# Kernel optimization log

Measured on AMD Instinct MI355X. Metric: run time of the kernel, lower is better.

## Reference

```python
import jax, jax.numpy as jnp
import numpy as np

MB, NK, DM, DT = 4096, 8, 1024, 128
EPS = 1e-3  # LayerNormalization eps, added to sigma OUTSIDE sqrt


def setup_inputs() -> dict:
    key = jax.random.key(0)
    ks = jax.random.split(key, 7)
    xav = lambda fan_in, fan_out: (2.0 / (fan_in + fan_out)) ** 0.5
    return {
        "q": jax.random.normal(ks[0], (MB, NK, DM), jnp.float32),
        "k": jax.random.normal(ks[1], (MB, NK, DM), jnp.float32),
        "v": jax.random.normal(ks[2], (MB, NK, DM), jnp.float32),
        "w_qs": jax.random.normal(ks[3], (NK, DM, DT), jnp.float32) * xav(DM, DT),
        "w_ks": jax.random.normal(ks[4], (NK, DM, DT), jnp.float32) * xav(DM, DT),
        "w_vs": jax.random.normal(ks[5], (NK, DM, DT), jnp.float32) * xav(DM, DT),
        # torch Linear: weight [out, in] = [NK*DM, NK*DT]
        "proj_w": jax.random.normal(ks[6], (NK * DM, NK * DT), jnp.float32) * xav(NK * DT, NK * DM),
        "proj_b": jnp.zeros((NK * DM,), jnp.float32),
        "gamma": jnp.ones((DM,), jnp.float32),
        "beta": jnp.zeros((DM,), jnp.float32),
    }


def reference(q, k, v, w_qs, w_ks, w_vs, proj_w, proj_b, gamma, beta):
    mb, nk, dm = q.shape
    dt = w_qs.shape[-1]
    residual = v

    # torch: q.view(n_kernel, mb, d_model) on contiguous [mb, nk, dm] == raw reshape
    q_s = jnp.einsum('nbd,ndt->nbt', q.reshape(nk, mb, dm), w_qs)  # [nk, mb, dt]
    k_s = jnp.einsum('nbd,ndt->nbt', k.reshape(nk, mb, dm), w_ks)
    v_s = jnp.einsum('nbd,ndt->nbt', v.reshape(nk, mb, dm), w_vs)

    # ScaledDotProductAttention on [nk*mb, 1, dt] -> scores [.,1,1]; softmax over
    # a singleton dim is identically 1, so output == v_s (faithful to source).
    temper = np.float32(np.sqrt(dm))
    scores = jnp.sum(q_s * k_s, axis=-1) / temper            # [nk, mb]
    attn = jax.nn.softmax(scores[:, :, None, None], axis=-1)  # [nk, mb, 1, 1] == 1.0
    out = attn[..., 0] * v_s                                  # [nk, mb, dt]
    attns = attn.reshape(nk * mb, 1, 1)

    # torch .view(mb, nk*dt) on the [nk, mb, dt]-contiguous buffer (raw reshape)
    outputs = out.reshape(mb, nk * dt)
    outputs = outputs @ proj_w.T + proj_b                     # [mb, nk*dm]
    z = outputs.reshape(mb, nk, dm) + residual

    # custom LayerNormalization: unbiased std, eps outside sqrt
    mu = jnp.mean(z, axis=-1, keepdims=True)
    sigma = jnp.std(z, axis=-1, keepdims=True, ddof=1)
    output = (z - mu) / (sigma + EPS) * gamma + beta
    return (output, attns)
```

## Files before the change

kernel.cpp:

```cpp
#include <hip/hip_runtime.h>
#include <cstdint>
#include <cstddef>

#define MB_   4096
#define NK_   8
#define DM_   1024
#define DT_   128

typedef __bf16 bf16;
typedef __bf16 bf16x8 __attribute__((ext_vector_type(8)));
typedef __bf16 bf16x4 __attribute__((ext_vector_type(4)));
typedef float  f32x4  __attribute__((ext_vector_type(4)));

__device__ __forceinline__ void gload_lds16(const void* g, void* l) {
  __builtin_amdgcn_global_load_lds(
      (__attribute__((address_space(1))) void*)g,
      (__attribute__((address_space(3))) void*)l,
      16, 0, 0);
}

__device__ __forceinline__ int hsw(int r) { return (r ^ (r >> 2)) & 3; }

__global__ void prep_pw_kernel(const float* __restrict__ pw, bf16* __restrict__ pwb) {
  size_t i = ((size_t)blockIdx.x * 256 + threadIdx.x) * 4;
  float4 f = *(const float4*)&pw[i];
  bf16x4 o = { (bf16)f.x, (bf16)f.y, (bf16)f.z, (bf16)f.w };
  *(bf16x4*)&pwb[i] = o;
}

__global__ void prep_wvt_kernel(const float* __restrict__ wvs, bf16* __restrict__ wvt) {
  int o = blockIdx.x * 256 + threadIdx.x;
  int d = o & 1023;
  int t = (o >> 10) & 127;
  int n = o >> 17;
  wvt[o] = (bf16)wvs[(size_t)n * 131072 + (size_t)d * 128 + t];
}

__global__ void fill_attns_kernel(float* __restrict__ out) {
  out[(size_t)33554432 + blockIdx.x * 256 + threadIdx.x] = 1.0f;
}

__global__ __launch_bounds__(256, 2) void gemm1_kernel(
    const float* __restrict__ vflat, const bf16* __restrict__ WvT,
    bf16* __restrict__ A2)
{
  __shared__ __align__(16) bf16 As[64 * 32];
  __shared__ __align__(16) bf16 Bs[128 * 32];
  const int tid  = threadIdx.x;
  const int wave = tid >> 6, lane = tid & 63;
  const int wm = wave >> 1, wn = wave & 1;
  const int n  = blockIdx.y;
  const int b0 = blockIdx.x * 64;

  const int r  = tid >> 2;
  const int hr = hsw(r);
  const int cs = (tid & 3) ^ hr;

  const float* ag = vflat + ((size_t)(n * MB_ + b0 + r)) * 1024 + (tid & 3) * 8;
  bf16* awr = As + r * 32 + cs * 8;
  const bf16* bg = WvT + (size_t)n * 131072 + (size_t)r * 1024 + cs * 8;
  char* bsb = (char*)Bs + wave * 1024;

  f32x4 acc[2][4] = {};
  const int krow = lane & 15;
  const int cch  = lane >> 4;
  const int swoff = ((cch ^ hsw(krow)) << 4);

  for (int kt = 0; kt < 32; ++kt) {
    const bf16* bptr = bg + kt * 32;
    gload_lds16(bptr,             bsb);
    gload_lds16(bptr + 64 * 1024, bsb + 4096);
    const float* aptr = ag + kt * 32;
    float4 f0 = *(const float4*)(aptr + 0);
    float4 f1 = *(const float4*)(aptr + 4);
    bf16x8 h0 = { (bf16)f0.x, (bf16)f0.y, (bf16)f0.z, (bf16)f0.w,
                  (bf16)f1.x, (bf16)f1.y, (bf16)f1.z, (bf16)f1.w };
    *(bf16x8*)awr = h0;
    __syncthreads();

    bf16x8 af[2], bfr[4];
    #pragma unroll
    for (int i = 0; i < 2; ++i)
      af[i] = *(const bf16x8*)((const char*)As + (wm * 32 + i * 16 + krow) * 64 + swoff);
    #pragma unroll
    for (int j = 0; j < 4; ++j)
      bfr[j] = *(const bf16x8*)((const char*)Bs + (wn * 64 + j * 16 + krow) * 64 + swoff);
    #pragma unroll
    for (int i = 0; i < 2; ++i)
      #pragma unroll
      for (int j = 0; j < 4; ++j)
        acc[i][j] = __builtin_amdgcn_mfma_f32_16x16x32_bf16(af[i], bfr[j], acc[i][j], 0, 0, 0);
    __syncthreads();
  }

  #pragma unroll
  for (int i = 0; i < 2; ++i) {
    #pragma unroll
    for (int j = 0; j < 4; ++j) {
      int t = wn * 64 + j * 16 + (lane & 15);
      #pragma unroll
      for (int rr = 0; rr < 4; ++rr) {
        int b = b0 + wm * 32 + i * 16 + (lane >> 4) * 4 + rr;
        size_t off = ((size_t)(n * 512 + (b >> 3))) * 1024 + (size_t)(b & 7) * 128 + t;
        A2[off] = (bf16)acc[i][j][rr];
      }
    }
  }
}

template<bool ZB>
__global__ __launch_bounds__(512, 2) void gemm2p_kernel(
    const bf16* __restrict__ A2, const bf16* __restrict__ PW,
    const float* __restrict__ pb, void* __restrict__ zoutp)
{
  __shared__ __align__(16) bf16 As[4][8192];
  __shared__ __align__(16) bf16 Bs[4][8192];

  const int tid  = threadIdx.x;
  const int w    = tid >> 6;
  const int lane = tid & 63;
  const int wm   = w >> 2;
  const int wn   = w & 3;

  const int bid   = blockIdx.x;
  const int x     = bid & 7;
  const int local = bid >> 3;
  const int mt    = local & 15;
  const int nt    = x * 4 + (local >> 4);
  const int m0    = mt * 256;
  const int n0    = nt * 256;

  const char* aG0 = (const char*)A2 + (size_t)(m0 + (tid >> 2)) * 2048 + (tid & 3) * 16;
  const char* aG1 = aG0 + (size_t)128 * 2048;
  const char* bG0 = (const char*)PW + (size_t)(n0 + (tid >> 2)) * 2048 + (tid & 3) * 16;
  const char* bG1 = bG0 + (size_t)128 * 2048;

  #define STAGE_A(t) { char* d = (char*)As[(t) & 3] + tid * 16;            \
                       gload_lds16(aG0 + (t) * 64, d);                      \
                       gload_lds16(aG1 + (t) * 64, d + 8192); }
  #define STAGE_B(t) { char* d = (char*)Bs[(t) & 3] + tid * 16;            \
                       gload_lds16(bG0 + (t) * 64, d);                      \
                       gload_lds16(bG1 + (t) * 64, d + 8192); }

  STAGE_A(0); STAGE_B(0); STAGE_A(1); STAGE_B(1);
  asm volatile("s_waitcnt vmcnt(4)" ::: "memory");
  __builtin_amdgcn_sched_barrier(0);
  __builtin_amdgcn_s_barrier();

  f32x4 acc[8][4] = {};
  const int fr = lane & 15;
  const int kc = (lane >> 4) * 8;
  const int aRd = (wm * 128 + fr) * 32 + kc;
  const int bRd = (wn * 64  + fr) * 32 + kc;

  #pragma unroll 4
  for (int t = 0; t < 32; ++t) {
    const bf16* pA = &As[t & 3][aRd];
    const bf16* pB = &Bs[t & 3][bRd];

    bf16x8 a[4], b[4];
    #pragma unroll
    for (int m = 0; m < 4; ++m) a[m] = *(const bf16x8*)(pA + m * 512);
    #pragma unroll
    for (int n = 0; n < 4; ++n) b[n] = *(const bf16x8*)(pB + n * 512);
    if (t < 30) STAGE_A(t + 2);
    __builtin_amdgcn_s_barrier();
    __builtin_amdgcn_s_setprio(1);
    #pragma unroll
    for (int m = 0; m < 4; ++m)
      #pragma unroll
      for (int n = 0; n < 4; ++n)
        acc[m][n] = __builtin_amdgcn_mfma_f32_16x16x32_bf16(a[m], b[n], acc[m][n], 0, 0, 0);
    __builtin_amdgcn_s_setprio(0);
    __builtin_amdgcn_s_barrier();

    bf16x8 a2[4];
    #pragma unroll
    for (int m = 0; m < 4; ++m) a2[m] = *(const bf16x8*)(pA + (4 + m) * 512);
    if (t < 30) STAGE_B(t + 2);
    __builtin_amdgcn_s_barrier();
    __builtin_amdgcn_s_setprio(1);
    #pragma unroll
    for (int m = 0; m < 4; ++m)
      #pragma unroll
      for (int n = 0; n < 4; ++n)
        acc[4 + m][n] = __builtin_amdgcn_mfma_f32_16x16x32_bf16(a2[m], b[n], acc[4 + m][n], 0, 0, 0);
    __builtin_amdgcn_s_setprio(0);
    if (t < 30)       { asm volatile("s_waitcnt vmcnt(4)" ::: "memory"); }
    else if (t == 30) { asm volatile("s_waitcnt vmcnt(0)" ::: "memory"); }
    __builtin_amdgcn_sched_barrier(0);
    __builtin_amdgcn_s_barrier();
  }
  #undef STAGE_A
  #undef STAGE_B

  #pragma unroll
  for (int m = 0; m < 8; ++m) {
    #pragma unroll
    for (int n = 0; n < 4; ++n) {
      int nn = n0 + wn * 64 + n * 16 + fr;
      float pbn = pb[nn];
      #pragma unroll
      for (int r = 0; r < 4; ++r) {
        int mm = m0 + wm * 128 + m * 16 + (lane >> 4) * 4 + r;
        size_t off = (size_t)mm * 8192 + nn;
        float val = acc[m][n][r] + pbn;
        if (ZB) ((bf16*)zoutp)[off] = (bf16)val;
        else    ((float*)zoutp)[off] = val;
      }
    }
  }
}

template<bool ZB>
__global__ __launch_bounds__(256) void ln_kernel(
    const void* zin, const float* __restrict__ vres,
    const float* __restrict__ gamma, const float* __restrict__ beta,
    float* outp)
{
  __shared__ float red[16];
  const int row = blockIdx.x;
  const int tid = threadIdx.x;
  const size_t base = (size_t)row * 1024 + tid * 4;

  float4 rv = *(const float4*)&vres[base];
  float4 x;
  if (ZB) {
    bf16x4 zb4 = *(const bf16x4*)((const bf16*)zin + base);
    x.x = (float)zb4[0] + rv.x; x.y = (float)zb4[1] + rv.y;
    x.z = (float)zb4[2] + rv.z; x.w = (float)zb4[3] + rv.w;
  } else {
    float4 zf = *(const float4*)((const float*)zin + base);
    x.x = zf.x + rv.x; x.y = zf.y + rv.y; x.z = zf.z + rv.z; x.w = zf.w + rv.w;
  }

  float s  = x.x + x.y + x.z + x.w;
  float ss = x.x * x.x + x.y * x.y + x.z * x.z + x.w * x.w;
  #pragma unroll
  for (int m = 32; m >= 1; m >>= 1) {
    s  += __shfl_xor(s,  m, 64);
    ss += __shfl_xor(ss, m, 64);
  }
  const int wave = tid >> 6, lane = tid & 63;
  if (lane == 0) { red[wave] = s; red[wave + 8] = ss; }
  __syncthreads();
  float S  = red[0] + red[1] + red[2] + red[3];
  float SS = red[8] + red[9] + red[10] + red[11];
  float mu  = S * (1.0f / 1024.0f);
  float var = (SS - 1024.0f * mu * mu) * (1.0f / 1023.0f);
  var = var < 0.0f ? 0.0f : var;
  float rs = 1.0f / (sqrtf(var) + 1e-3f);
  float4 g  = *(const float4*)&gamma[tid * 4];
  float4 be = *(const float4*)&beta[tid * 4];
  float4 y;
  y.x = (x.x - mu) * rs * g.x + be.x;
  y.y = (x.y - mu) * rs * g.y + be.y;
  y.z = (x.z - mu) * rs * g.z + be.z;
  y.w = (x.w - mu) * rs * g.w + be.w;
  *(float4*)&outp[base] = y;
}

extern "C" void kernel_launch(void* const* d_in, const int* in_sizes, int n_in,
                              void* d_out, int out_size, void* d_ws, size_t ws_size,
                              hipStream_t stream) {
  const float* v     = (const float*)d_in[2];
  const float* wvs   = (const float*)d_in[5];
  const float* pw    = (const float*)d_in[6];
  const float* pb    = (const float*)d_in[7];
  const float* gamma = (const float*)d_in[8];
  const float* beta  = (const float*)d_in[9];
  float* out = (float*)d_out;

  const size_t OFF_WVT = 16777216;
  const size_t OFF_A2  = OFF_WVT + 2097152;
  const size_t OFF_ZG  = OFF_A2 + 8388608;
  const size_t NEED_ZB = OFF_ZG + 67108864;

  bf16* PWb = (bf16*)d_ws;
  bf16* WvT = (bf16*)((char*)d_ws + OFF_WVT);
  bf16* A2  = (bf16*)((char*)d_ws + OFF_A2);
  const bool zb = (ws_size >= NEED_ZB);
  void* zbuf = zb ? (void*)((char*)d_ws + OFF_ZG) : (void*)out;

  hipLaunchKernelGGL(prep_pw_kernel,    dim3(8192), dim3(256), 0, stream, pw, PWb);
  hipLaunchKernelGGL(prep_wvt_kernel,   dim3(4096), dim3(256), 0, stream, wvs, WvT);
  hipLaunchKernelGGL(fill_attns_kernel, dim3(128),  dim3(256), 0, stream, out);
  hipLaunchKernelGGL(gemm1_kernel, dim3(64, 8), dim3(256), 0, stream, v, WvT, A2);
  if (zb) {
    hipLaunchKernelGGL((gemm2p_kernel<true>),  dim3(512), dim3(512), 0, stream, A2, PWb, pb, zbuf);
    hipLaunchKernelGGL((ln_kernel<true>),      dim3(32768), dim3(256), 0, stream, zbuf, v, gamma, beta, out);
  } else {
    hipLaunchKernelGGL((gemm2p_kernel<false>), dim3(512), dim3(512), 0, stream, A2, PWb, pb, zbuf);
    hipLaunchKernelGGL((ln_kernel<false>),     dim3(32768), dim3(256), 0, stream, zbuf, v, gamma, beta, out);
  }
}
```

Baseline: 202.6 us.

## Fuse residual add and LayerNorm statistics into GEMM2 epilogue, swizzle LDS, deepen pipeline

The GEMM2 epilogue now adds bias and the residual v, and computes per-row partial sum and sum-of-squares for each 256-column tile through shuffles and an LDS reduction. It writes these to a stats buffer so the LayerNorm kernel only applies normalization and no longer reads v or reduces. Separately, LDS staging uses an XOR swizzle to reduce bank conflicts, and prefetch depth grows from 2 to 3 stages. The residual read moves into the GEMM epilogue with a strided access pattern. The statistics are also computed on fp32 values before bf16 rounding, so they differ slightly from the rounded values later normalized.

```diff
diff --git a/kernel.cpp b/kernel.cpp
--- a/kernel.cpp
+++ b/kernel.cpp
@@ -111,7 +111,8 @@
 template<bool ZB>
 __global__ __launch_bounds__(512, 2) void gemm2p_kernel(
     const bf16* __restrict__ A2, const bf16* __restrict__ PW,
-    const float* __restrict__ pb, void* __restrict__ zoutp)
+    const float* __restrict__ vres, const float* __restrict__ pb,
+    void* __restrict__ xoutp, float2* __restrict__ stats)
 {
   __shared__ __align__(16) bf16 As[4][8192];
   __shared__ __align__(16) bf16 Bs[4][8192];
@@ -130,9 +131,11 @@
   const int m0    = mt * 256;
   const int n0    = nt * 256;
 
-  const char* aG0 = (const char*)A2 + (size_t)(m0 + (tid >> 2)) * 2048 + (tid & 3) * 16;
+  const int rS = tid >> 2;
+  const int cS = (tid & 3) ^ hsw(rS);
+  const char* aG0 = (const char*)A2 + (size_t)(m0 + rS) * 2048 + cS * 16;
   const char* aG1 = aG0 + (size_t)128 * 2048;
-  const char* bG0 = (const char*)PW + (size_t)(n0 + (tid >> 2)) * 2048 + (tid & 3) * 16;
+  const char* bG0 = (const char*)PW + (size_t)(n0 + rS) * 2048 + cS * 16;
   const char* bG1 = bG0 + (size_t)128 * 2048;
 
   #define STAGE_A(t) { char* d = (char*)As[(t) & 3] + tid * 16;            \
@@ -142,28 +145,29 @@
                        gload_lds16(bG0 + (t) * 64, d);                      \
                        gload_lds16(bG1 + (t) * 64, d + 8192); }
 
-  STAGE_A(0); STAGE_B(0); STAGE_A(1); STAGE_B(1);
-  asm volatile("s_waitcnt vmcnt(4)" ::: "memory");
+  STAGE_A(0); STAGE_B(0); STAGE_A(1); STAGE_B(1); STAGE_A(2); STAGE_B(2);
+  asm volatile("s_waitcnt vmcnt(8)" ::: "memory");
   __builtin_amdgcn_sched_barrier(0);
   __builtin_amdgcn_s_barrier();
 
   f32x4 acc[8][4] = {};
   const int fr = lane & 15;
-  const int kc = (lane >> 4) * 8;
-  const int aRd = (wm * 128 + fr) * 32 + kc;
-  const int bRd = (wn * 64  + fr) * 32 + kc;
+  const int g  = lane >> 4;
+  const int swoff = ((g ^ hsw(fr)) << 4);
+  const int aRd = (wm * 128 + fr) * 64 + swoff;
+  const int bRd = (wn * 64  + fr) * 64 + swoff;
 
   #pragma unroll 4
   for (int t = 0; t < 32; ++t) {
-    const bf16* pA = &As[t & 3][aRd];
-    const bf16* pB = &Bs[t & 3][bRd];
+    const char* pA = (const char*)As[t & 3] + aRd;
+    const char* pB = (const char*)Bs[t & 3] + bRd;
 
     bf16x8 a[4], b[4];
     #pragma unroll
-    for (int m = 0; m < 4; ++m) a[m] = *(const bf16x8*)(pA + m * 512);
-    #pragma unroll
-    for (int n = 0; n < 4; ++n) b[n] = *(const bf16x8*)(pB + n * 512);
-    if (t < 30) STAGE_A(t + 2);
+    for (int m = 0; m < 4; ++m) a[m] = *(const bf16x8*)(pA + m * 1024);
+    #pragma unroll
+    for (int n = 0; n < 4; ++n) b[n] = *(const bf16x8*)(pB + n * 1024);
+    if (t < 29) STAGE_A(t + 3);
     __builtin_amdgcn_s_barrier();
     __builtin_amdgcn_s_setprio(1);
     #pragma unroll
@@ -176,8 +180,8 @@
 
     bf16x8 a2[4];
     #pragma unroll
-    for (int m = 0; m < 4; ++m) a2[m] = *(const bf16x8*)(pA + (4 + m) * 512);
-    if (t < 30) STAGE_B(t + 2);
+    for (int m = 0; m < 4; ++m) a2[m] = *(const bf16x8*)(pA + (4 + m) * 1024);
+    if (t < 29) STAGE_B(t + 3);
     __builtin_amdgcn_s_barrier();
     __builtin_amdgcn_s_setprio(1);
     #pragma unroll
@@ -186,7 +190,8 @@
       for (int n = 0; n < 4; ++n)
         acc[4 + m][n] = __builtin_amdgcn_mfma_f32_16x16x32_bf16(a2[m], b[n], acc[4 + m][n], 0, 0, 0);
     __builtin_amdgcn_s_setprio(0);
-    if (t < 30)       { asm volatile("s_waitcnt vmcnt(4)" ::: "memory"); }
+    if (t < 29)       { asm volatile("s_waitcnt vmcnt(8)" ::: "memory"); }
+    else if (t == 29) { asm volatile("s_waitcnt vmcnt(4)" ::: "memory"); }
     else if (t == 30) { asm volatile("s_waitcnt vmcnt(0)" ::: "memory"); }
     __builtin_amdgcn_sched_barrier(0);
     __builtin_amdgcn_s_barrier();
@@ -194,69 +199,107 @@
   #undef STAGE_A
   #undef STAGE_B
 
+  float pbv[4];
+  #pragma unroll
+  for (int n = 0; n < 4; ++n) pbv[n] = pb[n0 + wn * 64 + n * 16 + fr];
+
+  float sthr[8][4], qthr[8][4];
   #pragma unroll
   for (int m = 0; m < 8; ++m) {
     #pragma unroll
+    for (int r = 0; r < 4; ++r) {
+      int lrow = wm * 128 + m * 16 + g * 4 + r;
+      const float* vrow = vres + (size_t)(m0 + lrow) * 8192 + n0 + wn * 64 + fr;
+      float s = 0.0f, q2 = 0.0f;
+      #pragma unroll
+      for (int n = 0; n < 4; ++n) {
+        float xv = acc[m][n][r] + pbv[n] + vrow[n * 16];
+        acc[m][n][r] = xv;
+        s += xv; q2 += xv * xv;
+      }
+      sthr[m][r] = s; qthr[m][r] = q2;
+    }
+  }
+  #pragma unroll
+  for (int m = 0; m < 8; ++m) {
+    #pragma unroll
     for (int n = 0; n < 4; ++n) {
-      int nn = n0 + wn * 64 + n * 16 + fr;
-      float pbn = pb[nn];
+      size_t coff = (size_t)(n0 + wn * 64 + n * 16 + fr);
       #pragma unroll
       for (int r = 0; r < 4; ++r) {
-        int mm = m0 + wm * 128 + m * 16 + (lane >> 4) * 4 + r;
-        size_t off = (size_t)mm * 8192 + nn;
-        float val = acc[m][n][r] + pbn;
-        if (ZB) ((bf16*)zoutp)[off] = (bf16)val;
-        else    ((float*)zoutp)[off] = val;
+        size_t off = (size_t)(m0 + wm * 128 + m * 16 + g * 4 + r) * 8192 + coff;
+        if (ZB) ((bf16*)xoutp)[off] = (bf16)acc[m][n][r];
+        else    ((float*)xoutp)[off] = acc[m][n][r];
       }
     }
   }
+  #pragma unroll
+  for (int m = 0; m < 8; ++m)
+    #pragma unroll
+    for (int r = 0; r < 4; ++r) {
+      float s = sthr[m][r], q2 = qthr[m][r];
+      #pragma unroll
+      for (int msk = 8; msk >= 1; msk >>= 1) {
+        s  += __shfl_xor(s,  msk, 64);
+        q2 += __shfl_xor(q2, msk, 64);
+      }
+      sthr[m][r] = s; qthr[m][r] = q2;
+    }
+  float* sredS = (float*)&As[0][0];
+  float* sredQ = sredS + 1024;
+  if (fr == 0) {
+    #pragma unroll
+    for (int m = 0; m < 8; ++m)
+      #pragma unroll
+      for (int r = 0; r < 4; ++r) {
+        int lrow = wm * 128 + m * 16 + g * 4 + r;
+        sredS[lrow * 4 + wn] = sthr[m][r];
+        sredQ[lrow * 4 + wn] = qthr[m][r];
+      }
+  }
+  __syncthreads();
+  if (tid < 256) {
+    float S  = sredS[tid * 4] + sredS[tid * 4 + 1] + sredS[tid * 4 + 2] + sredS[tid * 4 + 3];
+    float SS = sredQ[tid * 4] + sredQ[tid * 4 + 1] + sredQ[tid * 4 + 2] + sredQ[tid * 4 + 3];
+    int rid = (m0 + tid) * 8 + (nt >> 2);
+    stats[(size_t)rid * 4 + (nt & 3)] = make_float2(S, SS);
+  }
 }
 
 template<bool ZB>
-__global__ __launch_bounds__(256) void ln_kernel(
-    const void* zin, const float* __restrict__ vres,
+__global__ __launch_bounds__(256) void ln_apply_kernel(
+    const void* xin, const float2* __restrict__ stats,
     const float* __restrict__ gamma, const float* __restrict__ beta,
     float* outp)
 {
-  __shared__ float red[16];
-  const int row = blockIdx.x;
+  const int bid = blockIdx.x;
   const int tid = threadIdx.x;
-  const size_t base = (size_t)row * 1024 + tid * 4;
-
-  float4 rv = *(const float4*)&vres[base];
-  float4 x;
-  if (ZB) {
-    bf16x4 zb4 = *(const bf16x4*)((const bf16*)zin + base);
-    x.x = (float)zb4[0] + rv.x; x.y = (float)zb4[1] + rv.y;
-    x.z = (float)zb4[2] + rv.z; x.w = (float)zb4[3] + rv.w;
-  } else {
-    float4 zf = *(const float4*)((const float*)zin + base);
-    x.x = zf.x + rv.x; x.y = zf.y + rv.y; x.z = zf.z + rv.z; x.w = zf.w + rv.w;
-  }
-
-  float s  = x.x + x.y + x.z + x.w;
-  float ss = x.x * x.x + x.y * x.y + x.z * x.z + x.w * x.w;
-  #pragma unroll
-  for (int m = 32; m >= 1; m >>= 1) {
-    s  += __shfl_xor(s,  m, 64);
-    ss += __shfl_xor(ss, m, 64);
-  }
-  const int wave = tid >> 6, lane = tid & 63;
-  if (lane == 0) { red[wave] = s; red[wave + 8] = ss; }
-  __syncthreads();
-  float S  = red[0] + red[1] + red[2] + red[3];
-  float SS = red[8] + red[9] + red[10] + red[11];
+  float2 st0 = stats[(size_t)bid * 4 + 0];
+  float2 st1 = stats[(size_t)bid * 4 + 1];
+  float2 st2 = stats[(size_t)bid * 4 + 2];
+  float2 st3 = stats[(size_t)bid * 4 + 3];
+  float S  = st0.x + st1.x + st2.x + st3.x;
+  float SS = st0.y + st1.y + st2.y + st3.y;
   float mu  = S * (1.0f / 1024.0f);
   float var = (SS - 1024.0f * mu * mu) * (1.0f / 1023.0f);
   var = var < 0.0f ? 0.0f : var;
   float rs = 1.0f / (sqrtf(var) + 1e-3f);
-  float4 g  = *(const float4*)&gamma[tid * 4];
+
+  const size_t base = (size_t)bid * 1024 + tid * 4;
+  float4 xv;
+  if (ZB) {
+    bf16x4 xb = *(const bf16x4*)((const bf16*)xin + base);
+    xv.x = (float)xb[0]; xv.y = (float)xb[1]; xv.z = (float)xb[2]; xv.w = (float)xb[3];
+  } else {
+    xv = *(const float4*)((const float*)xin + base);
+  }
+  float4 ga = *(const float4*)&gamma[tid * 4];
   float4 be = *(const float4*)&beta[tid * 4];
   float4 y;
-  y.x = (x.x - mu) * rs * g.x + be.x;
-  y.y = (x.y - mu) * rs * g.y + be.y;
-  y.z = (x.z - mu) * rs * g.z + be.z;
-  y.w = (x.w - mu) * rs * g.w + be.w;
+  y.x = (xv.x - mu) * rs * ga.x + be.x;
+  y.y = (xv.y - mu) * rs * ga.y + be.y;
+  y.z = (xv.z - mu) * rs * ga.z + be.z;
+  y.w = (xv.w - mu) * rs * ga.w + be.w;
   *(float4*)&outp[base] = y;
 }
 
@@ -273,24 +316,30 @@
 
   const size_t OFF_WVT = 16777216;
   const size_t OFF_A2  = OFF_WVT + 2097152;
-  const size_t OFF_ZG  = OFF_A2 + 8388608;
-  const size_t NEED_ZB = OFF_ZG + 67108864;
-
-  bf16* PWb = (bf16*)d_ws;
-  bf16* WvT = (bf16*)((char*)d_ws + OFF_WVT);
-  bf16* A2  = (bf16*)((char*)d_ws + OFF_A2);
+  const size_t OFF_ST  = OFF_A2 + 8388608;
+  const size_t OFF_X   = OFF_ST + 1048576;
+  const size_t NEED_ZB = OFF_X + 67108864;
+
+  bf16*   PWb   = (bf16*)d_ws;
+  bf16*   WvT   = (bf16*)((char*)d_ws + OFF_WVT);
+  bf16*   A2    = (bf16*)((char*)d_ws + OFF_A2);
+  float2* stats = (float2*)((char*)d_ws + OFF_ST);
   const bool zb = (ws_size >= NEED_ZB);
-  void* zbuf = zb ? (void*)((char*)d_ws + OFF_ZG) : (void*)out;
+  void* xbuf = zb ? (void*)((char*)d_ws + OFF_X) : (void*)out;
 
   hipLaunchKernelGGL(prep_pw_kernel,    dim3(8192), dim3(256), 0, stream, pw, PWb);
   hipLaunchKernelGGL(prep_wvt_kernel,   dim3(4096), dim3(256), 0, stream, wvs, WvT);
   hipLaunchKernelGGL(fill_attns_kernel, dim3(128),  dim3(256), 0, stream, out);
   hipLaunchKernelGGL(gemm1_kernel, dim3(64, 8), dim3(256), 0, stream, v, WvT, A2);
   if (zb) {
-    hipLaunchKernelGGL((gemm2p_kernel<true>),  dim3(512), dim3(512), 0, stream, A2, PWb, pb, zbuf);
-    hipLaunchKernelGGL((ln_kernel<true>),      dim3(32768), dim3(256), 0, stream, zbuf, v, gamma, beta, out);
+    hipLaunchKernelGGL((gemm2p_kernel<true>),  dim3(512), dim3(512), 0, stream,
+                       A2, PWb, v, pb, xbuf, stats);
+    hipLaunchKernelGGL((ln_apply_kernel<true>),  dim3(32768), dim3(256), 0, stream,
+                       xbuf, stats, gamma, beta, out);
   } else {
-    hipLaunchKernelGGL((gemm2p_kernel<false>), dim3(512), dim3(512), 0, stream, A2, PWb, pb, zbuf);
-    hipLaunchKernelGGL((ln_kernel<false>),     dim3(32768), dim3(256), 0, stream, zbuf, v, gamma, beta, out);
-  }
-}
+    hipLaunchKernelGGL((gemm2p_kernel<false>), dim3(512), dim3(512), 0, stream,
+                       A2, PWb, v, pb, xbuf, stats);
+    hipLaunchKernelGGL((ln_apply_kernel<false>), dim3(32768), dim3(256), 0, stream,
+                       xbuf, stats, gamma, beta, out);
+  }
+}
```

Result: slower. 214.6 us (+5.9%).

## Swizzle LDS tiles and deepen prefetch pipeline in projection GEMM

Applied to the files above, without the earlier changes.

The projection GEMM now XOR-swizzles the 16-byte column chunks it fetches from global memory into LDS. The fragment reads apply the matching swizzle, which is meant to remove LDS bank conflicts on the bf16x8 loads. The prefetch depth goes from two to three K-tiles in flight. The main loop now processes two tiles per iteration in MFMA quarter blocks, with the global-to-LDS issues spread between them, to hide load latency better. The cost is more barriers per tile and tighter waitcnt bookkeeping near the loop tail.

```diff
diff --git a/kernel.cpp b/kernel.cpp
--- a/kernel.cpp
+++ b/kernel.cpp
@@ -109,9 +109,9 @@
 }
 
 template<bool ZB>
-__global__ __launch_bounds__(512, 2) void gemm2p_kernel(
+__global__ __launch_bounds__(512, 2) void gemm2p8_kernel(
     const bf16* __restrict__ A2, const bf16* __restrict__ PW,
-    const float* __restrict__ pb, void* __restrict__ zoutp)
+    const float* __restrict__ pb, void* __restrict__ xoutp)
 {
   __shared__ __align__(16) bf16 As[4][8192];
   __shared__ __align__(16) bf16 Bs[4][8192];
@@ -130,69 +130,121 @@
   const int m0    = mt * 256;
   const int n0    = nt * 256;
 
-  const char* aG0 = (const char*)A2 + (size_t)(m0 + (tid >> 2)) * 2048 + (tid & 3) * 16;
+  const int rS = tid >> 2;
+  const int cS = (tid & 3) ^ hsw(rS);
+  const char* aG0 = (const char*)A2 + (size_t)(m0 + rS) * 2048 + cS * 16;
   const char* aG1 = aG0 + (size_t)128 * 2048;
-  const char* bG0 = (const char*)PW + (size_t)(n0 + (tid >> 2)) * 2048 + (tid & 3) * 16;
+  const char* bG0 = (const char*)PW + (size_t)(n0 + rS) * 2048 + cS * 16;
   const char* bG1 = bG0 + (size_t)128 * 2048;
 
-  #define STAGE_A(t) { char* d = (char*)As[(t) & 3] + tid * 16;            \
-                       gload_lds16(aG0 + (t) * 64, d);                      \
-                       gload_lds16(aG1 + (t) * 64, d + 8192); }
-  #define STAGE_B(t) { char* d = (char*)Bs[(t) & 3] + tid * 16;            \
-                       gload_lds16(bG0 + (t) * 64, d);                      \
-                       gload_lds16(bG1 + (t) * 64, d + 8192); }
-
-  STAGE_A(0); STAGE_B(0); STAGE_A(1); STAGE_B(1);
-  asm volatile("s_waitcnt vmcnt(4)" ::: "memory");
+  #define SA0(t) gload_lds16(aG0 + (size_t)(t) * 64, (char*)As[(t) & 3] + tid * 16)
+  #define SA1(t) gload_lds16(aG1 + (size_t)(t) * 64, (char*)As[(t) & 3] + 8192 + tid * 16)
+  #define SB0(t) gload_lds16(bG0 + (size_t)(t) * 64, (char*)Bs[(t) & 3] + tid * 16)
+  #define SB1(t) gload_lds16(bG1 + (size_t)(t) * 64, (char*)Bs[(t) & 3] + 8192 + tid * 16)
+
+  SA0(0); SA1(0); SB0(0); SB1(0);
+  SA0(1); SA1(1); SB0(1); SB1(1);
+  SA0(2); SA1(2); SB0(2); SB1(2);
+  asm volatile("s_waitcnt vmcnt(8)" ::: "memory");
   __builtin_amdgcn_sched_barrier(0);
   __builtin_amdgcn_s_barrier();
 
   f32x4 acc[8][4] = {};
   const int fr = lane & 15;
-  const int kc = (lane >> 4) * 8;
-  const int aRd = (wm * 128 + fr) * 32 + kc;
-  const int bRd = (wn * 64  + fr) * 32 + kc;
-
-  #pragma unroll 4
-  for (int t = 0; t < 32; ++t) {
-    const bf16* pA = &As[t & 3][aRd];
-    const bf16* pB = &Bs[t & 3][bRd];
-
+  const int g  = lane >> 4;
+  const int swoff = ((g ^ hsw(fr)) << 4);
+  const int aRd = (wm * 128 + fr) * 64 + swoff;
+  const int bRd = (wn * 64  + fr) * 64 + swoff;
+
+  #define MFMA_Q(MB, NB)                                                     \
+    { __builtin_amdgcn_s_setprio(1);                                         \
+      _Pragma("unroll")                                                      \
+      for (int m = 0; m < 4; ++m) {                                          \
+        _Pragma("unroll")                                                    \
+        for (int n = 0; n < 2; ++n)                                          \
+          acc[(MB) + m][(NB) + n] = __builtin_amdgcn_mfma_f32_16x16x32_bf16( \
+              a[m], b[(NB) + n], acc[(MB) + m][(NB) + n], 0, 0, 0);          \
+      }                                                                      \
+      __builtin_amdgcn_s_setprio(0); }
+
+  #pragma unroll 1
+  for (int i = 0; i < 16; ++i) {
+    const int t0 = 2 * i, t1 = 2 * i + 1;
+    const int sA = t0 + 3, sB = t0 + 4;
+    const bool doA = (sA < 32), doB = (sB < 32);
+    const char* pA0 = (const char*)As[t0 & 3] + aRd;
+    const char* pB0 = (const char*)Bs[t0 & 3] + bRd;
+    const char* pA1 = (const char*)As[t1 & 3] + aRd;
+    const char* pB1 = (const char*)Bs[t1 & 3] + bRd;
     bf16x8 a[4], b[4];
-    #pragma unroll
-    for (int m = 0; m < 4; ++m) a[m] = *(const bf16x8*)(pA + m * 512);
-    #pragma unroll
-    for (int n = 0; n < 4; ++n) b[n] = *(const bf16x8*)(pB + n * 512);
-    if (t < 30) STAGE_A(t + 2);
-    __builtin_amdgcn_s_barrier();
-    __builtin_amdgcn_s_setprio(1);
-    #pragma unroll
-    for (int m = 0; m < 4; ++m)
-      #pragma unroll
-      for (int n = 0; n < 4; ++n)
-        acc[m][n] = __builtin_amdgcn_mfma_f32_16x16x32_bf16(a[m], b[n], acc[m][n], 0, 0, 0);
-    __builtin_amdgcn_s_setprio(0);
-    __builtin_amdgcn_s_barrier();
-
-    bf16x8 a2[4];
-    #pragma unroll
-    for (int m = 0; m < 4; ++m) a2[m] = *(const bf16x8*)(pA + (4 + m) * 512);
-    if (t < 30) STAGE_B(t + 2);
-    __builtin_amdgcn_s_barrier();
-    __builtin_amdgcn_s_setprio(1);
-    #pragma unroll
-    for (int m = 0; m < 4; ++m)
-      #pragma unroll
-      for (int n = 0; n < 4; ++n)
-        acc[4 + m][n] = __builtin_amdgcn_mfma_f32_16x16x32_bf16(a2[m], b[n], acc[4 + m][n], 0, 0, 0);
-    __builtin_amdgcn_s_setprio(0);
-    if (t < 30)       { asm volatile("s_waitcnt vmcnt(4)" ::: "memory"); }
-    else if (t == 30) { asm volatile("s_waitcnt vmcnt(0)" ::: "memory"); }
+
+    #pragma unroll
+    for (int m = 0; m < 4; ++m) a[m] = *(const bf16x8*)(pA0 + m * 1024);
+    #pragma unroll
+    for (int n = 0; n < 2; ++n) b[n] = *(const bf16x8*)(pB0 + n * 1024);
+    if (doA) SA0(sA);
+    __builtin_amdgcn_s_barrier();
+    MFMA_Q(0, 0);
+    __builtin_amdgcn_s_barrier();
+
+    #pragma unroll
+    for (int n = 0; n < 2; ++n) b[2 + n] = *(const bf16x8*)(pB0 + (2 + n) * 1024);
+    if (doA) SA1(sA);
+    __builtin_amdgcn_s_barrier();
+    MFMA_Q(0, 2);
+    __builtin_amdgcn_s_barrier();
+
+    #pragma unroll
+    for (int m = 0; m < 4; ++m) a[m] = *(const bf16x8*)(pA0 + (4 + m) * 1024);
+    if (doA) SB0(sA);
+    __builtin_amdgcn_s_barrier();
+    MFMA_Q(4, 0);
+    __builtin_amdgcn_s_barrier();
+
+    if (doA) SB1(sA);
+    if (i < 15) { asm volatile("s_waitcnt vmcnt(8)" ::: "memory"); }
+    else        { asm volatile("s_waitcnt vmcnt(0)" ::: "memory"); }
     __builtin_amdgcn_sched_barrier(0);
     __builtin_amdgcn_s_barrier();
-  }
-  #undef STAGE_A
-  #undef STAGE_B
+    MFMA_Q(4, 2);
+    __builtin_amdgcn_s_barrier();
+
+    #pragma unroll
+    for (int m = 0; m < 4; ++m) a[m] = *(const bf16x8*)(pA1 + m * 1024);
+    #pragma unroll
+    for (int n = 0; n < 2; ++n) b[n] = *(const bf16x8*)(pB1 + n * 1024);
+    if (doB) SA0(sB);
+    __builtin_amdgcn_s_barrier();
+    MFMA_Q(0, 0);
+    __builtin_amdgcn_s_barrier();
+
+    #pragma unroll
+    for (int n = 0; n < 2; ++n) b[2 + n] = *(const bf16x8*)(pB1 + (2 + n) * 1024);
+    if (doB) SA1(sB);
+    __builtin_amdgcn_s_barrier();
+    MFMA_Q(0, 2);
+    __builtin_amdgcn_s_barrier();
+
+    #pragma unroll
+    for (int m = 0; m < 4; ++m) a[m] = *(const bf16x8*)(pA1 + (4 + m) * 1024);
+    if (doB) SB0(sB);
+    __builtin_amdgcn_s_barrier();
+    MFMA_Q(4, 0);
+    __builtin_amdgcn_s_barrier();
+
+    if (doB) SB1(sB);
+    if (i < 14)      { asm volatile("s_waitcnt vmcnt(8)" ::: "memory"); }
+    else if (i == 14){ asm volatile("s_waitcnt vmcnt(4)" ::: "memory"); }
+    __builtin_amdgcn_sched_barrier(0);
+    __builtin_amdgcn_s_barrier();
+    MFMA_Q(4, 2);
+    __builtin_amdgcn_s_barrier();
+  }
+  #undef SA0
+  #undef SA1
+  #undef SB0
+  #undef SB1
+  #undef MFMA_Q
 
   #pragma unroll
   for (int m = 0; m < 8; ++m) {
@@ -202,11 +254,11 @@
       float pbn = pb[nn];
       #pragma unroll
       for (int r = 0; r < 4; ++r) {
-        int mm = m0 + wm * 128 + m * 16 + (lane >> 4) * 4 + r;
+        int mm = m0 + wm * 128 + m * 16 + g * 4 + r;
         size_t off = (size_t)mm * 8192 + nn;
         float val = acc[m][n][r] + pbn;
-        if (ZB) ((bf16*)zoutp)[off] = (bf16)val;
-        else    ((float*)zoutp)[off] = val;
+        if (ZB) ((bf16*)xoutp)[off] = (bf16)val;
+        else    ((float*)xoutp)[off] = val;
       }
     }
   }
@@ -250,13 +302,13 @@
   float var = (SS - 1024.0f * mu * mu) * (1.0f / 1023.0f);
   var = var < 0.0f ? 0.0f : var;
   float rs = 1.0f / (sqrtf(var) + 1e-3f);
-  float4 g  = *(const float4*)&gamma[tid * 4];
-  float4 be = *(const float4*)&beta[tid * 4];
+  float4 gmv = *(const float4*)&gamma[tid * 4];
+  float4 be  = *(const float4*)&beta[tid * 4];
   float4 y;
-  y.x = (x.x - mu) * rs * g.x + be.x;
-  y.y = (x.y - mu) * rs * g.y + be.y;
-  y.z = (x.z - mu) * rs * g.z + be.z;
-  y.w = (x.w - mu) * rs * g.w + be.w;
+  y.x = (x.x - mu) * rs * gmv.x + be.x;
+  y.y = (x.y - mu) * rs * gmv.y + be.y;
+  y.z = (x.z - mu) * rs * gmv.z + be.z;
+  y.w = (x.w - mu) * rs * gmv.w + be.w;
   *(float4*)&outp[base] = y;
 }
 
@@ -273,24 +325,24 @@
 
   const size_t OFF_WVT = 16777216;
   const size_t OFF_A2  = OFF_WVT + 2097152;
-  const size_t OFF_ZG  = OFF_A2 + 8388608;
-  const size_t NEED_ZB = OFF_ZG + 67108864;
+  const size_t OFF_X   = OFF_A2 + 8388608;
+  const size_t NEED_ZB = OFF_X + 67108864;
 
   bf16* PWb = (bf16*)d_ws;
   bf16* WvT = (bf16*)((char*)d_ws + OFF_WVT);
   bf16* A2  = (bf16*)((char*)d_ws + OFF_A2);
   const bool zb = (ws_size >= NEED_ZB);
-  void* zbuf = zb ? (void*)((char*)d_ws + OFF_ZG) : (void*)out;
+  void* xbuf = zb ? (void*)((char*)d_ws + OFF_X) : (void*)out;
 
   hipLaunchKernelGGL(prep_pw_kernel,    dim3(8192), dim3(256), 0, stream, pw, PWb);
   hipLaunchKernelGGL(prep_wvt_kernel,   dim3(4096), dim3(256), 0, stream, wvs, WvT);
   hipLaunchKernelGGL(fill_attns_kernel, dim3(128),  dim3(256), 0, stream, out);
   hipLaunchKernelGGL(gemm1_kernel, dim3(64, 8), dim3(256), 0, stream, v, WvT, A2);
   if (zb) {
-    hipLaunchKernelGGL((gemm2p_kernel<true>),  dim3(512), dim3(512), 0, stream, A2, PWb, pb, zbuf);
-    hipLaunchKernelGGL((ln_kernel<true>),      dim3(32768), dim3(256), 0, stream, zbuf, v, gamma, beta, out);
+    hipLaunchKernelGGL((gemm2p8_kernel<true>),  dim3(512), dim3(512), 0, stream, A2, PWb, pb, xbuf);
+    hipLaunchKernelGGL((ln_kernel<true>),       dim3(32768), dim3(256), 0, stream, xbuf, v, gamma, beta, out);
   } else {
-    hipLaunchKernelGGL((gemm2p_kernel<false>), dim3(512), dim3(512), 0, stream, A2, PWb, pb, zbuf);
-    hipLaunchKernelGGL((ln_kernel<false>),     dim3(32768), dim3(256), 0, stream, zbuf, v, gamma, beta, out);
-  }
-}
+    hipLaunchKernelGGL((gemm2p8_kernel<false>), dim3(512), dim3(512), 0, stream, A2, PWb, pb, xbuf);
+    hipLaunchKernelGGL((ln_kernel<false>),      dim3(32768), dim3(256), 0, stream, xbuf, v, gamma, beta, out);
+  }
+}
```

New measurement: 201.0 us. About the same (-0.8%).

## Restructure projection GEMM pipeline with swizzled LDS, deeper prefetch, and merged prep kernels

Applied to the files above, without the earlier changes.

The projection GEMM now XOR-swizzles the 16-byte chunks it loads into LDS to cut bank conflicts. It prefetches three stages ahead with a single combined A/B stage per iteration, so each iteration does one barrier instead of four and issues all 32 MFMAs at once. The two weight-conversion kernels are merged into one launch, and the attention-ones fill is folded into the layernorm kernel, removing two launches. In exchange, holding all 8 A fragments per iteration raises register pressure, and the setprio hints are dropped.

```diff
diff --git a/kernel.cpp b/kernel.cpp
--- a/kernel.cpp
+++ b/kernel.cpp
@@ -21,23 +21,21 @@
 
 __device__ __forceinline__ int hsw(int r) { return (r ^ (r >> 2)) & 3; }
 
-__global__ void prep_pw_kernel(const float* __restrict__ pw, bf16* __restrict__ pwb) {
-  size_t i = ((size_t)blockIdx.x * 256 + threadIdx.x) * 4;
-  float4 f = *(const float4*)&pw[i];
-  bf16x4 o = { (bf16)f.x, (bf16)f.y, (bf16)f.z, (bf16)f.w };
-  *(bf16x4*)&pwb[i] = o;
-}
-
-__global__ void prep_wvt_kernel(const float* __restrict__ wvs, bf16* __restrict__ wvt) {
-  int o = blockIdx.x * 256 + threadIdx.x;
-  int d = o & 1023;
-  int t = (o >> 10) & 127;
-  int n = o >> 17;
-  wvt[o] = (bf16)wvs[(size_t)n * 131072 + (size_t)d * 128 + t];
-}
-
-__global__ void fill_attns_kernel(float* __restrict__ out) {
-  out[(size_t)33554432 + blockIdx.x * 256 + threadIdx.x] = 1.0f;
+__global__ void prep_kernel(const float* __restrict__ pw, bf16* __restrict__ pwb,
+                            const float* __restrict__ wvs, bf16* __restrict__ wvt) {
+  int b = blockIdx.x;
+  if (b < 8192) {
+    size_t i = ((size_t)b * 256 + threadIdx.x) * 4;
+    float4 f = *(const float4*)&pw[i];
+    bf16x4 o = { (bf16)f.x, (bf16)f.y, (bf16)f.z, (bf16)f.w };
+    *(bf16x4*)&pwb[i] = o;
+  } else {
+    int o = (b - 8192) * 256 + threadIdx.x;
+    int d = o & 1023;
+    int t = (o >> 10) & 127;
+    int n = o >> 17;
+    wvt[o] = (bf16)wvs[(size_t)n * 131072 + (size_t)d * 128 + t];
+  }
 }
 
 __global__ __launch_bounds__(256, 2) void gemm1_kernel(
@@ -109,9 +107,9 @@
 }
 
 template<bool ZB>
-__global__ __launch_bounds__(512, 2) void gemm2p_kernel(
+__global__ __launch_bounds__(512, 2) void gemm2c_kernel(
     const bf16* __restrict__ A2, const bf16* __restrict__ PW,
-    const float* __restrict__ pb, void* __restrict__ zoutp)
+    const float* __restrict__ pb, void* __restrict__ xoutp)
 {
   __shared__ __align__(16) bf16 As[4][8192];
   __shared__ __align__(16) bf16 Bs[4][8192];
@@ -130,69 +128,57 @@
   const int m0    = mt * 256;
   const int n0    = nt * 256;
 
-  const char* aG0 = (const char*)A2 + (size_t)(m0 + (tid >> 2)) * 2048 + (tid & 3) * 16;
+  const int rS = tid >> 2;
+  const int cS = (tid & 3) ^ hsw(rS);
+  const char* aG0 = (const char*)A2 + (size_t)(m0 + rS) * 2048 + cS * 16;
   const char* aG1 = aG0 + (size_t)128 * 2048;
-  const char* bG0 = (const char*)PW + (size_t)(n0 + (tid >> 2)) * 2048 + (tid & 3) * 16;
+  const char* bG0 = (const char*)PW + (size_t)(n0 + rS) * 2048 + cS * 16;
   const char* bG1 = bG0 + (size_t)128 * 2048;
 
-  #define STAGE_A(t) { char* d = (char*)As[(t) & 3] + tid * 16;            \
-                       gload_lds16(aG0 + (t) * 64, d);                      \
-                       gload_lds16(aG1 + (t) * 64, d + 8192); }
-  #define STAGE_B(t) { char* d = (char*)Bs[(t) & 3] + tid * 16;            \
-                       gload_lds16(bG0 + (t) * 64, d);                      \
-                       gload_lds16(bG1 + (t) * 64, d + 8192); }
-
-  STAGE_A(0); STAGE_B(0); STAGE_A(1); STAGE_B(1);
-  asm volatile("s_waitcnt vmcnt(4)" ::: "memory");
+  #define STAGE(t) { char* dA = (char*)As[(t) & 3] + tid * 16;               \
+                     char* dB = (char*)Bs[(t) & 3] + tid * 16;               \
+                     gload_lds16(aG0 + (size_t)(t) * 64, dA);                \
+                     gload_lds16(aG1 + (size_t)(t) * 64, dA + 8192);         \
+                     gload_lds16(bG0 + (size_t)(t) * 64, dB);                \
+                     gload_lds16(bG1 + (size_t)(t) * 64, dB + 8192); }
+
+  STAGE(0); STAGE(1); STAGE(2);
+  asm volatile("s_waitcnt vmcnt(8)" ::: "memory");
+  __builtin_amdgcn_s_barrier();
   __builtin_amdgcn_sched_barrier(0);
-  __builtin_amdgcn_s_barrier();
 
   f32x4 acc[8][4] = {};
   const int fr = lane & 15;
-  const int kc = (lane >> 4) * 8;
-  const int aRd = (wm * 128 + fr) * 32 + kc;
-  const int bRd = (wn * 64  + fr) * 32 + kc;
-
-  #pragma unroll 4
-  for (int t = 0; t < 32; ++t) {
-    const bf16* pA = &As[t & 3][aRd];
-    const bf16* pB = &Bs[t & 3][bRd];
-
-    bf16x8 a[4], b[4];
-    #pragma unroll
-    for (int m = 0; m < 4; ++m) a[m] = *(const bf16x8*)(pA + m * 512);
-    #pragma unroll
-    for (int n = 0; n < 4; ++n) b[n] = *(const bf16x8*)(pB + n * 512);
-    if (t < 30) STAGE_A(t + 2);
-    __builtin_amdgcn_s_barrier();
-    __builtin_amdgcn_s_setprio(1);
-    #pragma unroll
-    for (int m = 0; m < 4; ++m)
+  const int g  = lane >> 4;
+  const int swoff = ((g ^ hsw(fr)) << 4);
+  const int aRd = (wm * 128 + fr) * 64 + swoff;
+  const int bRd = (wn * 64  + fr) * 64 + swoff;
+
+  #pragma unroll 1
+  for (int s = 0; s < 32; ++s) {
+    if (s < 29) STAGE(s + 3);
+
+    const char* pA = (const char*)As[s & 3] + aRd;
+    const char* pB = (const char*)Bs[s & 3] + bRd;
+    bf16x8 a[8], b[4];
+    #pragma unroll
+    for (int m = 0; m < 8; ++m) a[m] = *(const bf16x8*)(pA + m * 1024);
+    #pragma unroll
+    for (int n = 0; n < 4; ++n) b[n] = *(const bf16x8*)(pB + n * 1024);
+    #pragma unroll
+    for (int m = 0; m < 8; ++m)
       #pragma unroll
       for (int n = 0; n < 4; ++n)
         acc[m][n] = __builtin_amdgcn_mfma_f32_16x16x32_bf16(a[m], b[n], acc[m][n], 0, 0, 0);
-    __builtin_amdgcn_s_setprio(0);
+
+    asm volatile("s_waitcnt lgkmcnt(0)" ::: "memory");
+    if (s < 29)       { asm volatile("s_waitcnt vmcnt(8)" ::: "memory"); }
+    else if (s == 29) { asm volatile("s_waitcnt vmcnt(4)" ::: "memory"); }
+    else if (s == 30) { asm volatile("s_waitcnt vmcnt(0)" ::: "memory"); }
     __builtin_amdgcn_s_barrier();
-
-    bf16x8 a2[4];
-    #pragma unroll
-    for (int m = 0; m < 4; ++m) a2[m] = *(const bf16x8*)(pA + (4 + m) * 512);
-    if (t < 30) STAGE_B(t + 2);
-    __builtin_amdgcn_s_barrier();
-    __builtin_amdgcn_s_setprio(1);
-    #pragma unroll
-    for (int m = 0; m < 4; ++m)
-      #pragma unroll
-      for (int n = 0; n < 4; ++n)
-        acc[4 + m][n] = __builtin_amdgcn_mfma_f32_16x16x32_bf16(a2[m], b[n], acc[4 + m][n], 0, 0, 0);
-    __builtin_amdgcn_s_setprio(0);
-    if (t < 30)       { asm volatile("s_waitcnt vmcnt(4)" ::: "memory"); }
-    else if (t == 30) { asm volatile("s_waitcnt vmcnt(0)" ::: "memory"); }
     __builtin_amdgcn_sched_barrier(0);
-    __builtin_amdgcn_s_barrier();
-  }
-  #undef STAGE_A
-  #undef STAGE_B
+  }
+  #undef STAGE
 
   #pragma unroll
   for (int m = 0; m < 8; ++m) {
@@ -202,11 +188,11 @@
       float pbn = pb[nn];
       #pragma unroll
       for (int r = 0; r < 4; ++r) {
-        int mm = m0 + wm * 128 + m * 16 + (lane >> 4) * 4 + r;
+        int mm = m0 + wm * 128 + m * 16 + g * 4 + r;
         size_t off = (size_t)mm * 8192 + nn;
         float val = acc[m][n][r] + pbn;
-        if (ZB) ((bf16*)zoutp)[off] = (bf16)val;
-        else    ((float*)zoutp)[off] = val;
+        if (ZB) ((bf16*)xoutp)[off] = (bf16)val;
+        else    ((float*)xoutp)[off] = val;
       }
     }
   }
@@ -221,6 +207,7 @@
   __shared__ float red[16];
   const int row = blockIdx.x;
   const int tid = threadIdx.x;
+  if (row < 128) outp[(size_t)33554432 + row * 256 + tid] = 1.0f;
   const size_t base = (size_t)row * 1024 + tid * 4;
 
   float4 rv = *(const float4*)&vres[base];
@@ -250,13 +237,13 @@
   float var = (SS - 1024.0f * mu * mu) * (1.0f / 1023.0f);
   var = var < 0.0f ? 0.0f : var;
   float rs = 1.0f / (sqrtf(var) + 1e-3f);
-  float4 g  = *(const float4*)&gamma[tid * 4];
-  float4 be = *(const float4*)&beta[tid * 4];
+  float4 gmv = *(const float4*)&gamma[tid * 4];
+  float4 be  = *(const float4*)&beta[tid * 4];
   float4 y;
-  y.x = (x.x - mu) * rs * g.x + be.x;
-  y.y = (x.y - mu) * rs * g.y + be.y;
-  y.z = (x.z - mu) * rs * g.z + be.z;
-  y.w = (x.w - mu) * rs * g.w + be.w;
+  y.x = (x.x - mu) * rs * gmv.x + be.x;
+  y.y = (x.y - mu) * rs * gmv.y + be.y;
+  y.z = (x.z - mu) * rs * gmv.z + be.z;
+  y.w = (x.w - mu) * rs * gmv.w + be.w;
   *(float4*)&outp[base] = y;
 }
 
@@ -273,24 +260,22 @@
 
   const size_t OFF_WVT = 16777216;
   const size_t OFF_A2  = OFF_WVT + 2097152;
-  const size_t OFF_ZG  = OFF_A2 + 8388608;
-  const size_t NEED_ZB = OFF_ZG + 67108864;
+  const size_t OFF_X   = OFF_A2 + 8388608;
+  const size_t NEED_ZB = OFF_X + 67108864;
 
   bf16* PWb = (bf16*)d_ws;
   bf16* WvT = (bf16*)((char*)d_ws + OFF_WVT);
   bf16* A2  = (bf16*)((char*)d_ws + OFF_A2);
   const bool zb = (ws_size >= NEED_ZB);
-  void* zbuf = zb ? (void*)((char*)d_ws + OFF_ZG) : (void*)out;
-
-  hipLaunchKernelGGL(prep_pw_kernel,    dim3(8192), dim3(256), 0, stream, pw, PWb);
-  hipLaunchKernelGGL(prep_wvt_kernel,   dim3(4096), dim3(256), 0, stream, wvs, WvT);
-  hipLaunchKernelGGL(fill_attns_kernel, dim3(128),  dim3(256), 0, stream, out);
+  void* xbuf = zb ? (void*)((char*)d_ws + OFF_X) : (void*)out;
+
+  hipLaunchKernelGGL(prep_kernel, dim3(12288), dim3(256), 0, stream, pw, PWb, wvs, WvT);
   hipLaunchKernelGGL(gemm1_kernel, dim3(64, 8), dim3(256), 0, stream, v, WvT, A2);
   if (zb) {
-    hipLaunchKernelGGL((gemm2p_kernel<true>),  dim3(512), dim3(512), 0, stream, A2, PWb, pb, zbuf);
-    hipLaunchKernelGGL((ln_kernel<true>),      dim3(32768), dim3(256), 0, stream, zbuf, v, gamma, beta, out);
+    hipLaunchKernelGGL((gemm2c_kernel<true>),  dim3(512), dim3(512), 0, stream, A2, PWb, pb, xbuf);
+    hipLaunchKernelGGL((ln_kernel<true>),      dim3(32768), dim3(256), 0, stream, xbuf, v, gamma, beta, out);
   } else {
-    hipLaunchKernelGGL((gemm2p_kernel<false>), dim3(512), dim3(512), 0, stream, A2, PWb, pb, zbuf);
-    hipLaunchKernelGGL((ln_kernel<false>),     dim3(32768), dim3(256), 0, stream, zbuf, v, gamma, beta, out);
-  }
-}
+    hipLaunchKernelGGL((gemm2c_kernel<false>), dim3(512), dim3(512), 0, stream, A2, PWb, pb, xbuf);
+    hipLaunchKernelGGL((ln_kernel<false>),     dim3(32768), dim3(256), 0, stream, xbuf, v, gamma, beta, out);
+  }
+}
```

After: 209.1 us. 1.03x slower.
